# Performance work log

Hardware: AMD Instinct MI355X
Metric: run time of the kernel (lower is better)

Reference implementation:

```python
import jax, jax.numpy as jnp
import numpy as np
import math

N_NODES = 10000
N_EDGES = 30000
N_FEAT = 128
N_GRAPHS = 50
HEADS = 8
OUT_DIM = 10


def _lin_params(key, fin, fout):
    kw, kb = jax.random.split(key)
    s = 1.0 / math.sqrt(fin)
    w = jax.random.uniform(kw, (fin, fout), jnp.float32, -s, s)
    b = jax.random.uniform(kb, (fout,), jnp.float32, -s, s)
    return w, b


def setup_inputs() -> dict:
    key = jax.random.key(0)
    ks = jax.random.split(key, 20)
    inp = {}
    inp["x"] = jax.random.normal(ks[0], (N_NODES, N_FEAT), jnp.float32)
    inp["edge_index"] = jax.random.randint(ks[1], (2, N_EDGES), 0, N_NODES)
    inp["batch"] = jnp.sort(jax.random.randint(ks[2], (N_NODES,), 0, N_GRAPHS))
    # (fin, out_channels) per layer; internal width = out_channels * HEADS
    dims = [(128, 512), (512, 256), (256, 64)]
    ki = 3
    for i, (fin, cout) in enumerate(dims, 1):
        hc = cout * HEADS
        inp[f"q{i}_w"], inp[f"q{i}_b"] = _lin_params(ks[ki], fin, hc); ki += 1
        inp[f"k{i}_w"], inp[f"k{i}_b"] = _lin_params(ks[ki], fin, hc); ki += 1
        inp[f"v{i}_w"], inp[f"v{i}_b"] = _lin_params(ks[ki], fin, hc); ki += 1
        inp[f"s{i}_w"], inp[f"s{i}_b"] = _lin_params(ks[ki], fin, cout); ki += 1
    inp["gate_w"], inp["gate_b"] = _lin_params(ks[ki], 64, 1); ki += 1
    inp["fc_w"], inp["fc_b"] = _lin_params(ks[ki], 64, OUT_DIM)
    return inp


def _tconv(x, src, dst, qw, qb, kw_, kb_, vw, vb, sw, sb):
    # PyG TransformerConv, heads=HEADS, concat=False (mean over heads), root_weight=True
    N = x.shape[0]
    hc = qw.shape[1]
    C = hc // HEADS
    q = (x @ qw + qb).reshape(N, HEADS, C)
    k = (x @ kw_ + kb_).reshape(N, HEADS, C)
    v = (x @ vw + vb).reshape(N, HEADS, C)
    # per-edge attention logits [E, H]
    alpha = (q[dst] * k[src]).sum(-1) * (1.0 / math.sqrt(C))
    # segment softmax over incoming edges of each destination node
    m = jax.ops.segment_max(alpha, dst, num_segments=N)
    ex = jnp.exp(alpha - m[dst])
    den = jax.ops.segment_sum(ex, dst, num_segments=N)
    w = ex / jnp.maximum(den[dst], 1e-16)
    agg = jax.ops.segment_sum(w[:, :, None] * v[src], dst, num_segments=N)  # [N,H,C]
    return agg.mean(axis=1) + x @ sw + sb


def reference(x, edge_index, batch,
              q1_w, q1_b, k1_w, k1_b, v1_w, v1_b, s1_w, s1_b,
              q2_w, q2_b, k2_w, k2_b, v2_w, v2_b, s2_w, s2_b,
              q3_w, q3_b, k3_w, k3_b, v3_w, v3_b, s3_w, s3_b,
              gate_w, gate_b, fc_w, fc_b):
    src, dst = edge_index[0], edge_index[1]
    h = jax.nn.elu(_tconv(x, src, dst, q1_w, q1_b, k1_w, k1_b, v1_w, v1_b, s1_w, s1_b))
    h = jax.nn.elu(_tconv(h, src, dst, q2_w, q2_b, k2_w, k2_b, v2_w, v2_b, s2_w, s2_b))
    h = jax.nn.elu(_tconv(h, src, dst, q3_w, q3_b, k3_w, k3_b, v3_w, v3_b, s3_w, s3_b))
    # GlobalAttention pooling: softmax(gate) within each graph, weighted sum
    gate = h @ gate_w + gate_b  # [N,1]
    gm = jax.ops.segment_max(gate, batch, num_segments=N_GRAPHS)
    ge = jnp.exp(gate - gm[batch])
    gd = jax.ops.segment_sum(ge, batch, num_segments=N_GRAPHS)
    g = ge / jnp.maximum(gd[batch], 1e-16)
    pooled = jax.ops.segment_sum(g * h, batch, num_segments=N_GRAPHS)  # [G,64]
    return pooled @ fc_w + fc_b
```

## Files before the change

kernel.cpp:

```cpp
#include <hip/hip_runtime.h>
#include <stdint.h>
#include <math.h>

#define NN 10000
#define NE 30000
#define NG 50
#define NH 8

typedef _Float16 f16;
typedef _Float16 f16x2 __attribute__((ext_vector_type(2)));
typedef _Float16 f16x4 __attribute__((ext_vector_type(4)));
typedef _Float16 f16x8 __attribute__((ext_vector_type(8)));
typedef float f32x4 __attribute__((ext_vector_type(4)));

__device__ inline void async16(f16* l, const f16* g) {
    __builtin_amdgcn_global_load_lds((const __attribute__((address_space(1))) void*)g,
                                     (__attribute__((address_space(3))) void*)l, 16, 0, 0);
}

__global__ void hist_kernel(const int* __restrict__ dst, int* __restrict__ deg, int E) {
    int e = blockIdx.x * blockDim.x + threadIdx.x;
    if (e < E) atomicAdd(&deg[dst[e]], 1);
}

__global__ __launch_bounds__(1024) void scan_goffs(const int* __restrict__ deg, int* __restrict__ offs,
                                                   int* __restrict__ cursor,
                                                   const int* __restrict__ batch, int* __restrict__ goffs) {
    if (blockIdx.x == 1) {
        int g = threadIdx.x;
        if (g > NG) return;
        int lo = 0, hi = NN;
        while (lo < hi) {
            int mid = (lo + hi) >> 1;
            if (batch[mid] < g) lo = mid + 1; else hi = mid;
        }
        goffs[g] = lo;
        return;
    }
    __shared__ int tot[1024];
    const int t = threadIdx.x;
    const int base = t * 10;
    int v[10];
    int s = 0;
#pragma unroll
    for (int i = 0; i < 10; ++i) {
        int idx = base + i;
        v[i] = (idx < NN) ? deg[idx] : 0;
        s += v[i];
    }
    tot[t] = s;
    __syncthreads();
    for (int d2 = 1; d2 < 1024; d2 <<= 1) {
        int add = (t >= d2) ? tot[t - d2] : 0;
        __syncthreads();
        tot[t] += add;
        __syncthreads();
    }
    int run = tot[t] - s;
    if (t == 0) offs[0] = 0;
#pragma unroll
    for (int i = 0; i < 10; ++i) {
        int idx = base + i;
        if (idx < NN) cursor[idx] = run;
        run += v[i];
        if (idx < NN) offs[idx + 1] = run;
    }
}

__global__ void scatter_kernel(const int* __restrict__ src, const int* __restrict__ dst,
                               int* __restrict__ cursor, int* __restrict__ srcCSR, int E) {
    int e = blockIdx.x * blockDim.x + threadIdx.x;
    if (e < E) {
        int p = atomicAdd(&cursor[dst[e]], 1);
        srcCSR[p] = src[e];
    }
}

__global__ void sort_csr(const int* __restrict__ offs, int* __restrict__ srcCSR) {
    int n = blockIdx.x * blockDim.x + threadIdx.x;
    if (n >= NN) return;
    int s = offs[n], e = offs[n + 1];
    for (int i = s + 1; i < e; ++i) {
        int v = srcCSR[i];
        int j = i - 1;
        while (j >= s && srcCSR[j] > v) { srcCSR[j + 1] = srcCSR[j]; --j; }
        srcCSR[j + 1] = v;
    }
}

__global__ void cvt3_kernel(const float* __restrict__ a, f16* __restrict__ ao, int na,
                            const float* __restrict__ b, f16* __restrict__ bo, int nb2,
                            const float* __restrict__ c, f16* __restrict__ co, int nc) {
    int i = blockIdx.x * blockDim.x + threadIdx.x;
    if (i < na) ao[i] = (f16)a[i];
    else if (i < na + nb2) { int j = i - na; bo[j] = (f16)b[j]; }
    else if (i < na + nb2 + nc) { int j = i - na - nb2; co[j] = (f16)c[j]; }
}

__global__ __launch_bounds__(256) void prep4t(const float* __restrict__ W0, int n0,
                                              const float* __restrict__ W1, int n1,
                                              const float* __restrict__ W2, int n2,
                                              const float* __restrict__ W3, int n3,
                                              const float* __restrict__ b0, const float* __restrict__ b1,
                                              const float* __restrict__ b2, const float* __restrict__ b3,
                                              f16* __restrict__ Bt, float* __restrict__ bias,
                                              int K, int Ntot) {
    __shared__ float tile[64][65];
    const int k0 = blockIdx.x * 64;
    const int nb = blockIdx.y * 64;
    const int tid = threadIdx.x;
    const int tn = tid & 63;
    const int t4 = tid >> 6;
#pragma unroll
    for (int i = 0; i < 16; ++i) {
        int kl = t4 + i * 4;
        int k = k0 + kl;
        int n = nb + tn;
        float w = 0.0f;
        int m = n;
        if (m < n0) w = W0[(size_t)k * n0 + m];
        else { m -= n0;
            if (m < n1) w = W1[(size_t)k * n1 + m];
            else { m -= n1;
                if (m < n2) w = W2[(size_t)k * n2 + m];
                else { m -= n2; if (m < n3) w = W3[(size_t)k * n3 + m]; }
            }
        }
        tile[kl][tn] = w;
    }
    if (blockIdx.x == 0 && t4 == 0) {
        int n = nb + tn;
        float bv = 0.0f;
        int m = n;
        if (m < n0) bv = b0[m];
        else { m -= n0;
            if (m < n1) bv = b1[m];
            else { m -= n1;
                if (m < n2) bv = b2[m];
                else { m -= n2; if (m < n3) bv = b3[m]; }
            }
        }
        bias[n] = bv;
    }
    __syncthreads();
#pragma unroll
    for (int i = 0; i < 16; ++i) {
        int nl = t4 + i * 4;
        Bt[(size_t)(nb + nl) * K + k0 + tn] = (f16)tile[tn][nl];
    }
}

__global__ __launch_bounds__(256) void prepU(const float* __restrict__ qw, const float* __restrict__ qb,
                                             const float* __restrict__ kw, const float* __restrict__ kb,
                                             f16* __restrict__ BtY, float* __restrict__ biasY,
                                             int fin, int hc, int C) {
    const int wid = blockIdx.x * 4 + ((int)threadIdx.x >> 6);
    const int lane = threadIdx.x & 63;
    if (wid >= fin * 16) return;
    const int k = wid >> 4;
    const int idx = wid & 15;
    const int h = idx & 7, isV = idx >> 3;
    const float* W = isV ? kw : qw;
    const float* bvec = isV ? qb : kb;
    float s = 0.0f;
    for (int c = lane; c < C; c += 64) s += W[(size_t)k * hc + h * C + c] * bvec[h * C + c];
#pragma unroll
    for (int o = 32; o > 0; o >>= 1) s += __shfl_down(s, o, 64);
    if (lane == 0) BtY[(size_t)(8 * fin + isV * 8 + h) * fin + k] = (f16)s;
    if (wid < 8) {
        float cc = 0.0f;
        for (int c = lane; c < C; c += 64) cc += qb[wid * C + c] * kb[wid * C + c];
#pragma unroll
        for (int o = 32; o > 0; o >>= 1) cc += __shfl_down(cc, o, 64);
        if (lane == 0) biasY[8 * fin + wid] = cc;
    }
}

__global__ __launch_bounds__(256) void prepZB(const float* __restrict__ vw, const float* __restrict__ sw,
                                              const float* __restrict__ vb, const float* __restrict__ sb,
                                              f16* __restrict__ Bt2, float* __restrict__ biasZ) {
    __shared__ f16 tile[32][65];
    const int k0 = blockIdx.x * 32, c0 = blockIdx.y * 64;
    const int tid = threadIdx.x;
#pragma unroll
    for (int i = 0; i < 8; ++i) {
        int idx = tid + i * 256;
        int kl = idx >> 6, cl = idx & 63;
        int k = k0 + kl, c = c0 + cl;
        float v = 0.0f;
        if (k < 1024)      v = vw[(size_t)(k & 127) * 4096 + (k >> 7) * 512 + c];
        else if (k < 1152) v = sw[(size_t)(k - 1024) * 512 + c];
        else if (k < 1160) v = vb[(k - 1152) * 512 + c];
        tile[kl][cl] = (f16)v;
    }
    if (blockIdx.x == 0 && tid < 64) biasZ[c0 + tid] = sb[c0 + tid];
    __syncthreads();
    const int cl = tid >> 2, kl = (tid & 3) * 8;
    f16x8 v;
#pragma unroll
    for (int t = 0; t < 8; ++t) v[t] = tile[kl + t][cl];
    *(f16x8*)(Bt2 + (size_t)(c0 + cl) * 1184 + k0 + kl) = v;
}

__global__ __launch_bounds__(256) void gemm128(const f16* __restrict__ A, int lda, int zA,
                                               const f16* __restrict__ Bt, int ldb, int zB,
                                               const float* __restrict__ bias,
                                               f16* __restrict__ C, int ldc, int zC,
                                               float* __restrict__ Sf,
                                               int M, int Np, int K, int hcS, int Sw, int act) {
    __shared__ f16 smem[24576];
    const int rm = blockIdx.x * 128;
    if (rm >= M) return;
    A  += (size_t)blockIdx.z * zA;
    Bt += (size_t)blockIdx.z * zB;
    C  += (size_t)blockIdx.z * zC;
    const int tid  = threadIdx.x;
    const int lane = tid & 63;
    const int wave = tid >> 6;
    const int l16  = lane & 15;
    const int quad = lane >> 4;
    const int cn   = blockIdx.y * 128;
    const int wrow = (wave >> 1) * 64;
    const int wcol = (wave & 1) * 64;

    const int rS  = tid >> 2;
    const int kc  = ((tid & 3) ^ ((tid >> 3) & 3)) << 3;
    int rowA0 = rm + rS;       if (rowA0 >= M) rowA0 = M - 1;
    int rowA1 = rm + rS + 64;  if (rowA1 >= M) rowA1 = M - 1;
    const f16* gA0 = A + (size_t)rowA0 * lda + kc;
    const f16* gA1 = A + (size_t)rowA1 * lda + kc;
    const f16* gB0 = Bt + (size_t)(cn + rS) * ldb + kc;
    const f16* gB1 = Bt + (size_t)(cn + rS + 64) * ldb + kc;

    const int swf = (l16 >> 1) & 3;
    const int rdAoff = (wrow + l16) * 32 + ((quad ^ swf) << 3);
    const int rdBoff = 4096 + (wcol + l16) * 32 + ((quad ^ swf) << 3);

    f32x4 acc[4][4] = {};

    auto stage_load = [&](int slot) {
        f16* base = smem + slot * 8192;
        async16(base + tid * 8, gA0);
        async16(base + tid * 8 + 2048, gA1);
        async16(base + 4096 + tid * 8, gB0);
        async16(base + 4096 + tid * 8 + 2048, gB1);
        gA0 += 32; gA1 += 32; gB0 += 32; gB1 += 32;
    };

    const int NI = K >> 5;
    stage_load(0);
    stage_load(1);

    int slot = 0;
    for (int i = 0; i < NI; ++i) {
        if (i + 1 < NI) asm volatile("s_waitcnt vmcnt(4)" ::: "memory");
        else            asm volatile("s_waitcnt vmcnt(0)" ::: "memory");
        asm volatile("s_barrier" ::: "memory");
        if (i + 2 < NI) {
            int s2 = slot + 2; if (s2 >= 3) s2 -= 3;
            stage_load(s2);
        }
        const f16* sb = smem + slot * 8192;
        f16x8 av[4], bv[4];
#pragma unroll
        for (int ii = 0; ii < 4; ++ii) av[ii] = *(const f16x8*)(sb + rdAoff + ii * 512);
#pragma unroll
        for (int j = 0; j < 4; ++j) bv[j] = *(const f16x8*)(sb + rdBoff + j * 512);
#pragma unroll
        for (int ii = 0; ii < 4; ++ii)
#pragma unroll
            for (int j = 0; j < 4; ++j)
                acc[ii][j] = __builtin_amdgcn_mfma_f32_16x16x32_f16(bv[j], av[ii], acc[ii][j], 0, 0, 0);
        ++slot; if (slot == 3) slot = 0;
    }
    __syncthreads();

    f16* sC = smem;
    for (int round = 0; round < 2; ++round) {
        if ((wave >> 1) == round) {
#pragma unroll
            for (int j = 0; j < 4; ++j) {
                const int cb = wcol + j * 16 + quad * 4;
                const float4 bb = *(const float4*)(bias + cn + cb);
#pragma unroll
                for (int i = 0; i < 4; ++i) {
                    const int r = i * 16 + l16;
                    float v0 = acc[i][j][0] + bb.x;
                    float v1 = acc[i][j][1] + bb.y;
                    float v2 = acc[i][j][2] + bb.z;
                    float v3 = acc[i][j][3] + bb.w;
                    if (act) {
                        v0 = v0 > 0.0f ? v0 : (__expf(v0) - 1.0f);
                        v1 = v1 > 0.0f ? v1 : (__expf(v1) - 1.0f);
                        v2 = v2 > 0.0f ? v2 : (__expf(v2) - 1.0f);
                        v3 = v3 > 0.0f ? v3 : (__expf(v3) - 1.0f);
                    }
                    f16x4 o;
                    o[0] = (f16)v0; o[1] = (f16)v1; o[2] = (f16)v2; o[3] = (f16)v3;
                    *(f16x4*)(sC + r * 136 + cb) = o;
                    if (Sf) {
                        const int sc = cn + cb - hcS;
                        if (sc >= 0 && sc < Sw) {
                            const int grow = rm + round * 64 + r;
                            if (grow < M) {
                                float4 sv = { v0, v1, v2, v3 };
                                *(float4*)(Sf + (size_t)grow * Sw + sc) = sv;
                            }
                        }
                    }
                }
            }
        }
        __syncthreads();
#pragma unroll
        for (int it = 0; it < 4; ++it) {
            const int r = it * 16 + (tid >> 4);
            const int ch = tid & 15;
            const int grow = rm + round * 64 + r;
            if (grow < M) {
                f16x8 v = *(const f16x8*)(sC + r * 136 + ch * 8);
                *(f16x8*)(C + (size_t)grow * ldc + cn + ch * 8) = v;
            }
        }
        __syncthreads();
    }
}

__global__ __launch_bounds__(256) void alpha_fused_y(const f16* __restrict__ Y, const f16* __restrict__ X,
                                                     const int* __restrict__ offs,
                                                     const int* __restrict__ srcCSR,
                                                     float* __restrict__ alphaW,
                                                     int strideY, int fin, float scale) {
    const int n = blockIdx.x;
    const int e0 = offs[n];
    int d = offs[n + 1] - e0;
    if (d > 256) d = 256;

    __shared__ __align__(16) f16 sy[1024];
    __shared__ float sew[256 * NH];
    __shared__ float sv[256 * NH];
    __shared__ int sed[256];
    __shared__ float su[NH];
    const int tid = threadIdx.x;

    const f16* Yn = Y + (size_t)n * strideY;
    for (int c = tid; c < fin; c += 256) ((f16x8*)sy)[c] = ((const f16x8*)Yn)[c];
    if (tid < NH) su[tid] = (float)Yn[8 * fin + tid];
    for (int e = tid; e < d; e += 256) {
        int s = srcCSR[e0 + e];
        sed[e] = s;
        f16x8 vv = *(const f16x8*)(Y + (size_t)s * strideY + 8 * fin + 8);
#pragma unroll
        for (int t = 0; t < 8; ++t) sv[e * NH + t] = (float)vv[t];
    }
    __syncthreads();

    const int wv = tid >> 6, lane = tid & 63;
    const int cph = fin >> 3;
    const int csh = __ffs(cph) - 1;
    const int passes = fin >> 6;
    for (int e = wv; e < d; e += 4) {
        const f16x8* kg = (const f16x8*)(X + (size_t)sed[e] * fin);
        for (int p = 0; p < passes; ++p) {
            const int ci = p * 64 + lane;
            const int head = ci >> csh;
            const int kcn = ci & (cph - 1);
            f16x8 yv = ((const f16x8*)sy)[ci];
            f16x8 xv = kg[kcn];
            float acc = 0.0f;
#pragma unroll
            for (int t = 0; t < 8; ++t) acc += (float)yv[t] * (float)xv[t];
            for (int o = cph >> 1; o > 0; o >>= 1) acc += __shfl_down(acc, o, cph);
            if ((lane & (cph - 1)) == 0)
                sew[e * NH + head] = (acc + su[head] + sv[e * NH + head]) * scale;
        }
    }
    __syncthreads();

    if (tid < NH) {
        const int h = tid;
        float m = -3.0e38f;
        for (int e = 0; e < d; ++e) m = fmaxf(m, sew[e * NH + h]);
        float den = 0.0f;
        for (int e = 0; e < d; ++e) {
            float ex = __expf(sew[e * NH + h] - m);
            sew[e * NH + h] = ex;
            den += ex;
        }
        float inv = 1.0f / (fmaxf(den, 1e-16f) * (float)NH);
        for (int e = 0; e < d; ++e) sew[e * NH + h] *= inv;
    }
    __syncthreads();

    for (int i = tid; i < d * NH; i += 256) alphaW[(size_t)e0 * NH + i] = sew[i];
}

__global__ __launch_bounds__(256) void z_agg(const f16* __restrict__ X,
                                             const int* __restrict__ offs,
                                             const int* __restrict__ srcCSR,
                                             const float* __restrict__ alphaW,
                                             f16* __restrict__ Z) {
    const int n = blockIdx.x;
    const int e0 = offs[n];
    int d = offs[n + 1] - e0;
    if (d > 256) d = 256;

    __shared__ float sew[256 * NH];
    __shared__ int sed[256];
    __shared__ __align__(16) f16 sx[32 * 128];
    const int tid = threadIdx.x;

    for (int i = tid; i < d * NH; i += 256) sew[i] = alphaW[(size_t)e0 * NH + i];
    for (int e = tid; e < d; e += 256) sed[e] = srcCSR[e0 + e];
    __syncthreads();

    const int h = tid >> 5;
    const int f0 = (tid * 4) & 127;
    float a0 = 0.0f, a1 = 0.0f, a2 = 0.0f, a3 = 0.0f;
    for (int ch = 0; ch < d; ch += 32) {
        const int cnt = min(32, d - ch);
        for (int idx = tid; idx < cnt * 16; idx += 256) {
            int row = idx >> 4, c8 = idx & 15;
            *(f16x8*)(sx + row * 128 + c8 * 8) = *(const f16x8*)(X + (size_t)sed[ch + row] * 128 + c8 * 8);
        }
        __syncthreads();
        for (int e = 0; e < cnt; ++e) {
            float w = sew[(ch + e) * NH + h];
            f16x4 xv = *(const f16x4*)(sx + e * 128 + f0);
            a0 += w * (float)xv[0];
            a1 += w * (float)xv[1];
            a2 += w * (float)xv[2];
            a3 += w * (float)xv[3];
        }
        __syncthreads();
    }
    f16* Zr = Z + (size_t)n * 1184;
    f16x4 o; o[0] = (f16)a0; o[1] = (f16)a1; o[2] = (f16)a2; o[3] = (f16)a3;
    *(f16x4*)(Zr + tid * 4) = o;
    if (tid < 16) *(f16x8*)(Zr + 1024 + tid * 8) = *(const f16x8*)(X + (size_t)n * 128 + tid * 8);
    if (tid >= 32 && tid < 40) {
        int hh = tid - 32;
        float s = 0.0f;
        for (int e = 0; e < d; ++e) s += sew[e * NH + hh];
        Zr[1152 + hh] = (f16)s;
    }
    if (tid >= 64 && tid < 88) Zr[1160 + (tid - 64)] = (f16)0.0f;
}

__global__ __launch_bounds__(256) void alpha_fused(const f16* __restrict__ QK,
                                                   const int* __restrict__ offs,
                                                   const int* __restrict__ srcCSR,
                                                   float* __restrict__ alphaW,
                                                   int strideQK, int C, int hc, float scale) {
    const int n = blockIdx.x;
    const int e0 = offs[n];
    int d = offs[n + 1] - e0;
    if (d > 256) d = 256;

    __shared__ __align__(16) f16 sq[4096];
    __shared__ float sew[256 * NH];
    __shared__ int sed[256];
    const int tid = threadIdx.x;

    const f16x8* qg = (const f16x8*)(QK + (size_t)n * strideQK);
    const int qchunks = hc >> 3;
    for (int c = tid; c < qchunks; c += 256) ((f16x8*)sq)[c] = qg[c];
    for (int e = tid; e < d; e += 256) sed[e] = srcCSR[e0 + e];
    __syncthreads();

    const int wv = tid >> 6, lane = tid & 63;
    const int cph = C >> 3;
    const int passes = hc >> 9;
    for (int e = wv; e < d; e += 4) {
        const f16x8* kg = (const f16x8*)(QK + (size_t)sed[e] * strideQK + hc);
        for (int p = 0; p < passes; ++p) {
            const int ci = p * 64 + lane;
            f16x8 qv = ((const f16x8*)sq)[ci];
            f16x8 kv = kg[ci];
            float acc = 0.0f;
#pragma unroll
            for (int t = 0; t < 8; ++t) acc += (float)qv[t] * (float)kv[t];
            for (int o = cph >> 1; o > 0; o >>= 1) acc += __shfl_down(acc, o, cph);
            if ((lane & (cph - 1)) == 0) {
                const int head = ci / cph;
                sew[e * NH + head] = acc * scale;
            }
        }
    }
    __syncthreads();

    if (tid < NH) {
        const int h = tid;
        float m = -3.0e38f;
        for (int e = 0; e < d; ++e) m = fmaxf(m, sew[e * NH + h]);
        float den = 0.0f;
        for (int e = 0; e < d; ++e) {
            float ex = __expf(sew[e * NH + h] - m);
            sew[e * NH + h] = ex;
            den += ex;
        }
        float inv = 1.0f / (fmaxf(den, 1e-16f) * (float)NH);
        for (int e = 0; e < d; ++e) sew[e * NH + h] *= inv;
    }
    __syncthreads();

    for (int i = tid; i < d * NH; i += 256) alphaW[(size_t)e0 * NH + i] = sew[i];
}

__global__ __launch_bounds__(256) void node_agg(const f16* __restrict__ VS,
                                                const float* __restrict__ Sf,
                                                const int* __restrict__ offs,
                                                const int* __restrict__ srcCSR,
                                                const float* __restrict__ alphaW,
                                                float* __restrict__ hout, f16* __restrict__ houth,
                                                int C, int NpVS, int writeHout) {
    const int n = blockIdx.x;
    const int e0 = offs[n];
    int d = offs[n + 1] - e0;
    if (d > 256) d = 256;

    __shared__ float sew[256 * NH];
    __shared__ int sed[256];
    __shared__ float sred[512];
    const int tid = threadIdx.x;

    for (int i = tid; i < d * NH; i += 256) sew[i] = alphaW[(size_t)e0 * NH + i];
    for (int e = tid; e < d; e += 256) sed[e] = srcCSR[e0 + e];
    __syncthreads();

    const int half = C >> 1;
    const int cp = tid & (half - 1);
    const int grp = tid / half;
    const int ngr = 256 / half;
    float a0 = 0.0f, a1 = 0.0f;
    for (int e = grp; e < d; e += ngr) {
        const unsigned int* vp = (const unsigned int*)(VS + (size_t)sed[e] * NpVS);
#pragma unroll
        for (int h = 0; h < NH; ++h) {
            float w = sew[e * NH + h];
            f16x2 vv = __builtin_bit_cast(f16x2, vp[((h * C) >> 1) + cp]);
            a0 += w * (float)vv.x;
            a1 += w * (float)vv.y;
        }
    }
    if (ngr > 1) {
        sred[tid] = a0;
        sred[256 + tid] = a1;
        __syncthreads();
        if (grp == 0) {
            for (int g = 1; g < ngr; ++g) {
                a0 += sred[g * half + cp];
                a1 += sred[256 + g * half + cp];
            }
        }
    }
    if (grp == 0) {
        const int c = cp * 2;
        const float* Sp = Sf + (size_t)n * C;
        float o0 = a0 + Sp[c];
        float o1 = a1 + Sp[c + 1];
        o0 = o0 > 0.0f ? o0 : (__expf(o0) - 1.0f);
        o1 = o1 > 0.0f ? o1 : (__expf(o1) - 1.0f);
        if (writeHout) {
            hout[(size_t)n * C + c] = o0;
            hout[(size_t)n * C + c + 1] = o1;
        }
        houth[(size_t)n * C + c] = (f16)o0;
        houth[(size_t)n * C + c + 1] = (f16)o1;
    }
}

__global__ __launch_bounds__(256) void pool_graph(const float* __restrict__ h,
                                                  const float* __restrict__ gw, const float* __restrict__ gb,
                                                  const float* __restrict__ fcw, const float* __restrict__ fcb,
                                                  const int* __restrict__ goffs,
                                                  float* __restrict__ gbuf, float* __restrict__ out) {
    const int g = blockIdx.x;
    const int s = goffs[g], e = goffs[g + 1];
    const int tid = threadIdx.x;
    const int wv = tid >> 6, lane = tid & 63;

    __shared__ float red[256];
    __shared__ float pl[64];
    __shared__ float sden;

    if (e == s) {
        if (tid < 10) out[g * 10 + tid] = fcb[tid];
        return;
    }

    const float gwl = gw[lane];
    for (int n = s + wv; n < e; n += 4) {
        float acc = h[(size_t)n * 64 + lane] * gwl;
#pragma unroll
        for (int o = 32; o > 0; o >>= 1) acc += __shfl_down(acc, o, 64);
        if (lane == 0) gbuf[n] = acc + gb[0];
    }
    __syncthreads();

    float m = -3.0e38f;
    for (int n = s + tid; n < e; n += 256) m = fmaxf(m, gbuf[n]);
    red[tid] = m;
    __syncthreads();
    for (int o = 128; o > 0; o >>= 1) {
        if (tid < o) red[tid] = fmaxf(red[tid], red[tid + o]);
        __syncthreads();
    }
    m = red[0];
    __syncthreads();

    float sum = 0.0f;
    for (int n = s + tid; n < e; n += 256) {
        float ex = __expf(gbuf[n] - m);
        gbuf[n] = ex;
        sum += ex;
    }
    red[tid] = sum;
    __syncthreads();
    for (int o = 128; o > 0; o >>= 1) {
        if (tid < o) red[tid] += red[tid + o];
        __syncthreads();
    }
    if (tid == 0) sden = 1.0f / fmaxf(red[0], 1e-16f);
    __syncthreads();

    float acc = 0.0f;
    for (int n = s + wv; n < e; n += 4) acc += gbuf[n] * h[(size_t)n * 64 + lane];
    red[tid] = acc;
    __syncthreads();
    if (wv == 0) pl[lane] = (red[lane] + red[64 + lane] + red[128 + lane] + red[192 + lane]) * sden;
    __syncthreads();

    if (tid < 10) {
        float o = fcb[tid];
#pragma unroll
        for (int c = 0; c < 64; ++c) o += pl[c] * fcw[c * 10 + tid];
        out[g * 10 + tid] = o;
    }
}

extern "C" void kernel_launch(void* const* d_in, const int* in_sizes, int n_in,
                              void* d_out, int out_size, void* d_ws, size_t ws_size,
                              hipStream_t stream) {
    const float* x   = (const float*)d_in[0];
    const int* ei    = (const int*)d_in[1];
    const int* src   = ei;
    const int* dst   = ei + NE;
    const int* batch = (const int*)d_in[2];

    struct LayerW { int fin, C, hc; const float *qw,*qb,*kw,*kb,*vw,*vb,*sw,*sb; };
    LayerW LW[3];
    const int fins[3] = {128, 512, 256};
    const int Cs[3]   = {512, 256, 64};
    for (int l = 0; l < 3; ++l) {
        int b = 3 + 8 * l;
        LW[l].fin = fins[l]; LW[l].C = Cs[l]; LW[l].hc = Cs[l] * NH;
        LW[l].qw = (const float*)d_in[b + 0]; LW[l].qb = (const float*)d_in[b + 1];
        LW[l].kw = (const float*)d_in[b + 2]; LW[l].kb = (const float*)d_in[b + 3];
        LW[l].vw = (const float*)d_in[b + 4]; LW[l].vb = (const float*)d_in[b + 5];
        LW[l].sw = (const float*)d_in[b + 6]; LW[l].sb = (const float*)d_in[b + 7];
    }
    const float* gate_w = (const float*)d_in[27];
    const float* gate_b = (const float*)d_in[28];
    const float* fc_w   = (const float*)d_in[29];
    const float* fc_b   = (const float*)d_in[30];

    size_t off = 0;
    char* ws = (char*)d_ws;
    auto alloc = [&](size_t bytes) -> void* {
        void* p = ws + off;
        off = (off + bytes + 255) & ~(size_t)255;
        return p;
    };
    f16* BtQK   = (f16*)alloc((size_t)6400 * 512 * sizeof(f16));
    f16* BtVS   = (f16*)alloc((size_t)512 * 1184 * sizeof(f16));
    float* biasQK = (float*)alloc(6400 * sizeof(float));
    float* biasVS = (float*)alloc(512 * sizeof(float));
    f16* QKbuf  = (f16*)alloc((size_t)NN * 6400 * sizeof(f16));
    float* Sf   = (float*)alloc((size_t)NN * 256 * sizeof(float));
    f16* xh     = (f16*)alloc((size_t)NN * 128 * sizeof(f16));
    f16* houth  = (f16*)alloc((size_t)NN * 512 * sizeof(f16));
    float* hf   = (float*)alloc((size_t)NN * 64 * sizeof(float));
    float* alphaW = (float*)alloc((size_t)NE * NH * sizeof(float));
    f16* qw16   = (f16*)alloc((size_t)128 * 4096 * sizeof(f16));
    f16* kw16   = (f16*)alloc((size_t)128 * 4096 * sizeof(f16));
    f16* BtY    = (f16*)alloc((size_t)1152 * 128 * sizeof(f16));
    int*   deg   = (int*)alloc(NN * sizeof(int));
    float* zbias = (float*)alloc(512 * sizeof(float));
    float* biasY = (float*)alloc(1152 * sizeof(float));
    size_t zspan = (size_t)((char*)(biasY + 1152) - (char*)deg);
    int* offs   = (int*)alloc((NN + 1) * sizeof(int));
    int* cursor = (int*)alloc(NN * sizeof(int));
    int* srcCSR = (int*)alloc(NE * sizeof(int));
    int* goffs  = (int*)alloc((NG + 1) * sizeof(int));
    float* gbuf = (float*)alloc(NN * sizeof(float));
    if (off > ws_size) return;

    hipMemsetAsync(deg, 0, zspan, stream);
    hist_kernel<<<(NE + 255) / 256, 256, 0, stream>>>(dst, deg, NE);
    scan_goffs<<<2, 1024, 0, stream>>>(deg, offs, cursor, batch, goffs);
    scatter_kernel<<<(NE + 255) / 256, 256, 0, stream>>>(src, dst, cursor, srcCSR, NE);
    sort_csr<<<(NN + 255) / 256, 256, 0, stream>>>(offs, srcCSR);

    {
        int na = NN * 128, nb2 = 128 * 4096, nc = 128 * 4096;
        cvt3_kernel<<<(na + nb2 + nc + 255) / 256, 256, 0, stream>>>(x, xh, na,
                                                                     LW[0].qw, qw16, nb2,
                                                                     LW[0].kw, kw16, nc);
    }

    const int grid_m = 80;
    const f16* Acur = xh;
    for (int l = 0; l < 3; ++l) {
        const int K = LW[l].fin, C = LW[l].C, hc = LW[l].hc;
        const float scale = 1.0f / sqrtf((float)C);

        if (l == 0) {
            const int fin = 128, NtotY = 1152;
            dim3 gm(1, 1, 8);
            gemm128<<<gm, 256, 0, stream>>>(kw16, hc, C, qw16, hc, C, zbias,
                                            BtY, fin, fin * fin, nullptr, fin, fin, C, 0, 0, 0);
            prepU<<<(fin * 16 + 3) / 4, 256, 0, stream>>>(LW[0].qw, LW[0].qb, LW[0].kw, LW[0].kb,
                                                          BtY, biasY, fin, hc, C);
            dim3 gy(grid_m, NtotY / 128);
            gemm128<<<gy, 256, 0, stream>>>(xh, fin, 0, BtY, fin, 0, biasY,
                                            QKbuf, NtotY, 0, nullptr, NN, NtotY, fin, 0, 0, 0);
            alpha_fused_y<<<NN, 256, 0, stream>>>(QKbuf, xh, offs, srcCSR, alphaW,
                                                  NtotY, fin, scale);
            z_agg<<<NN, 256, 0, stream>>>(xh, offs, srcCSR, alphaW, QKbuf);
            prepZB<<<dim3(37, 8), 256, 0, stream>>>(LW[0].vw, LW[0].sw, LW[0].vb, LW[0].sb,
                                                    BtVS, biasVS);
            dim3 gz(grid_m, 4);
            gemm128<<<gz, 256, 0, stream>>>(QKbuf, 1184, 0, BtVS, 1184, 0, biasVS,
                                            houth, 512, 0, nullptr, NN, 512, 1184, 0, 0, 1);
        } else {
            const int Np = (2 * hc + hc + C + 127) & ~127;
            prep4t<<<dim3(K / 64, Np / 64), 256, 0, stream>>>(LW[l].qw, hc, LW[l].kw, hc,
                                                              LW[l].vw, hc, LW[l].sw, C,
                                                              LW[l].qb, LW[l].kb, LW[l].vb, LW[l].sb,
                                                              BtQK, biasQK, K, Np);
            dim3 gq(grid_m, Np / 128);
            gemm128<<<gq, 256, 0, stream>>>(Acur, K, 0, BtQK, K, 0, biasQK,
                                            QKbuf, Np, 0, Sf, NN, Np, K, 3 * hc, C, 0);
            alpha_fused<<<NN, 256, 0, stream>>>(QKbuf, offs, srcCSR, alphaW, Np, C, hc, scale);
            node_agg<<<NN, 256, 0, stream>>>(QKbuf + 2 * hc, Sf, offs, srcCSR, alphaW, hf, houth,
                                             C, Np, l == 2 ? 1 : 0);
        }
        Acur = houth;
    }

    pool_graph<<<NG, 256, 0, stream>>>(hf, gate_w, gate_b, fc_w, fc_b, goffs, gbuf, (float*)d_out);
}
```

Before: 493.0 us.

## Fuse per-node attention softmax with aggregation and batch weight prep

```diff
diff --git a/kernel.cpp b/kernel.cpp
--- a/kernel.cpp
+++ b/kernel.cpp
@@ -97,14 +97,24 @@
     else if (i < na + nb2 + nc) { int j = i - na - nb2; co[j] = (f16)c[j]; }
 }
 
-__global__ __launch_bounds__(256) void prep4t(const float* __restrict__ W0, int n0,
-                                              const float* __restrict__ W1, int n1,
-                                              const float* __restrict__ W2, int n2,
-                                              const float* __restrict__ W3, int n3,
-                                              const float* __restrict__ b0, const float* __restrict__ b1,
-                                              const float* __restrict__ b2, const float* __restrict__ b3,
-                                              f16* __restrict__ Bt, float* __restrict__ bias,
-                                              int K, int Ntot) {
+__global__ __launch_bounds__(256) void prep4t2(
+        const float* W0a, int n0a, const float* W1a, int n1a,
+        const float* W2a, int n2a, const float* W3a, int n3a,
+        const float* b0a, const float* b1a, const float* b2a, const float* b3a,
+        f16* Bta, float* biasa, int Ka, int Na,
+        const float* W0b, int n0b, const float* W1b, int n1b,
+        const float* W2b, int n2b, const float* W3b, int n3b,
+        const float* b0b, const float* b1b, const float* b2b, const float* b3b,
+        f16* Btb, float* biasb, int Kb, int Nb) {
+    const int z = blockIdx.z;
+    const float *W0 = z ? W0b : W0a, *W1 = z ? W1b : W1a, *W2 = z ? W2b : W2a, *W3 = z ? W3b : W3a;
+    const float *b0 = z ? b0b : b0a, *b1 = z ? b1b : b1a, *b2 = z ? b2b : b2a, *b3 = z ? b3b : b3a;
+    const int n0 = z ? n0b : n0a, n1 = z ? n1b : n1a, n2 = z ? n2b : n2a, n3 = z ? n3b : n3a;
+    const int K = z ? Kb : Ka, Ntot = z ? Nb : Na;
+    f16* Bt = z ? Btb : Bta;
+    float* bias = z ? biasb : biasa;
+    if ((int)blockIdx.x * 64 >= K || (int)blockIdx.y * 64 >= Ntot) return;
+
     __shared__ float tile[64][65];
     const int k0 = blockIdx.x * 64;
     const int nb = blockIdx.y * 64;
@@ -326,11 +336,12 @@
     }
 }
 
-__global__ __launch_bounds__(256) void alpha_fused_y(const f16* __restrict__ Y, const f16* __restrict__ X,
-                                                     const int* __restrict__ offs,
-                                                     const int* __restrict__ srcCSR,
-                                                     float* __restrict__ alphaW,
-                                                     int strideY, int fin, float scale) {
+__global__ __launch_bounds__(256) void alpha_zagg(const f16* __restrict__ Y, const f16* __restrict__ X,
+                                                  const int* __restrict__ offs,
+                                                  const int* __restrict__ srcCSR,
+                                                  f16* __restrict__ Z,
+                                                  int strideY, float scale) {
+    const int fin = 128;
     const int n = blockIdx.x;
     const int e0 = offs[n];
     int d = offs[n + 1] - e0;
@@ -341,6 +352,7 @@
     __shared__ float sv[256 * NH];
     __shared__ int sed[256];
     __shared__ float su[NH];
+    __shared__ __align__(16) f16 sx[32 * 128];
     const int tid = threadIdx.x;
 
     const f16* Yn = Y + (size_t)n * strideY;
@@ -355,24 +367,25 @@
     }
     __syncthreads();
 
-    const int wv = tid >> 6, lane = tid & 63;
-    const int cph = fin >> 3;
-    const int csh = __ffs(cph) - 1;
-    const int passes = fin >> 6;
-    for (int e = wv; e < d; e += 4) {
-        const f16x8* kg = (const f16x8*)(X + (size_t)sed[e] * fin);
-        for (int p = 0; p < passes; ++p) {
-            const int ci = p * 64 + lane;
-            const int head = ci >> csh;
-            const int kcn = ci & (cph - 1);
-            f16x8 yv = ((const f16x8*)sy)[ci];
-            f16x8 xv = kg[kcn];
-            float acc = 0.0f;
-#pragma unroll
-            for (int t = 0; t < 8; ++t) acc += (float)yv[t] * (float)xv[t];
-            for (int o = cph >> 1; o > 0; o >>= 1) acc += __shfl_down(acc, o, cph);
-            if ((lane & (cph - 1)) == 0)
-                sew[e * NH + head] = (acc + su[head] + sv[e * NH + head]) * scale;
+    {
+        const int wv = tid >> 6, lane = tid & 63;
+        for (int e = wv; e < d; e += 4) {
+            const f16x8* kg = (const f16x8*)(X + (size_t)sed[e] * fin);
+#pragma unroll
+            for (int p = 0; p < 2; ++p) {
+                const int ci = p * 64 + lane;
+                const int head = ci >> 4;
+                const int kcn = ci & 15;
+                f16x8 yv = ((const f16x8*)sy)[ci];
+                f16x8 xv = kg[kcn];
+                float acc = 0.0f;
+#pragma unroll
+                for (int t = 0; t < 8; ++t) acc += (float)yv[t] * (float)xv[t];
+#pragma unroll
+                for (int o = 8; o > 0; o >>= 1) acc += __shfl_down(acc, o, 16);
+                if ((lane & 15) == 0)
+                    sew[e * NH + head] = (acc + su[head] + sv[e * NH + head]) * scale;
+            }
         }
     }
     __syncthreads();
@@ -392,28 +405,6 @@
     }
     __syncthreads();
 
-    for (int i = tid; i < d * NH; i += 256) alphaW[(size_t)e0 * NH + i] = sew[i];
-}
-
-__global__ __launch_bounds__(256) void z_agg(const f16* __restrict__ X,
-                                             const int* __restrict__ offs,
-                                             const int* __restrict__ srcCSR,
-                                             const float* __restrict__ alphaW,
-                                             f16* __restrict__ Z) {
-    const int n = blockIdx.x;
-    const int e0 = offs[n];
-    int d = offs[n + 1] - e0;
-    if (d > 256) d = 256;
-
-    __shared__ float sew[256 * NH];
-    __shared__ int sed[256];
-    __shared__ __align__(16) f16 sx[32 * 128];
-    const int tid = threadIdx.x;
-
-    for (int i = tid; i < d * NH; i += 256) sew[i] = alphaW[(size_t)e0 * NH + i];
-    for (int e = tid; e < d; e += 256) sed[e] = srcCSR[e0 + e];
-    __syncthreads();
-
     const int h = tid >> 5;
     const int f0 = (tid * 4) & 127;
     float a0 = 0.0f, a1 = 0.0f, a2 = 0.0f, a3 = 0.0f;
@@ -447,11 +438,12 @@
     if (tid >= 64 && tid < 88) Zr[1160 + (tid - 64)] = (f16)0.0f;
 }
 
-__global__ __launch_bounds__(256) void alpha_fused(const f16* __restrict__ QK,
-                                                   const int* __restrict__ offs,
-                                                   const int* __restrict__ srcCSR,
-                                                   float* __restrict__ alphaW,
-                                                   int strideQK, int C, int hc, float scale) {
+__global__ __launch_bounds__(256) void edge_node(const f16* __restrict__ QKVS,
+                                                 const float* __restrict__ Sf,
+                                                 const int* __restrict__ offs,
+                                                 const int* __restrict__ srcCSR,
+                                                 float* __restrict__ hout, f16* __restrict__ houth,
+                                                 int Np, int C, int hc, float scale, int writeHout) {
     const int n = blockIdx.x;
     const int e0 = offs[n];
     int d = offs[n + 1] - e0;
@@ -460,30 +452,33 @@
     __shared__ __align__(16) f16 sq[4096];
     __shared__ float sew[256 * NH];
     __shared__ int sed[256];
+    __shared__ float sred[512];
     const int tid = threadIdx.x;
 
-    const f16x8* qg = (const f16x8*)(QK + (size_t)n * strideQK);
+    const f16x8* qg = (const f16x8*)(QKVS + (size_t)n * Np);
     const int qchunks = hc >> 3;
     for (int c = tid; c < qchunks; c += 256) ((f16x8*)sq)[c] = qg[c];
     for (int e = tid; e < d; e += 256) sed[e] = srcCSR[e0 + e];
     __syncthreads();
 
-    const int wv = tid >> 6, lane = tid & 63;
-    const int cph = C >> 3;
-    const int passes = hc >> 9;
-    for (int e = wv; e < d; e += 4) {
-        const f16x8* kg = (const f16x8*)(QK + (size_t)sed[e] * strideQK + hc);
-        for (int p = 0; p < passes; ++p) {
-            const int ci = p * 64 + lane;
-            f16x8 qv = ((const f16x8*)sq)[ci];
-            f16x8 kv = kg[ci];
-            float acc = 0.0f;
-#pragma unroll
-            for (int t = 0; t < 8; ++t) acc += (float)qv[t] * (float)kv[t];
-            for (int o = cph >> 1; o > 0; o >>= 1) acc += __shfl_down(acc, o, cph);
-            if ((lane & (cph - 1)) == 0) {
-                const int head = ci / cph;
-                sew[e * NH + head] = acc * scale;
+    {
+        const int wv = tid >> 6, lane = tid & 63;
+        const int cph = C >> 3;
+        const int passes = (hc >> 9) ? (hc >> 9) : 1;
+        for (int e = wv; e < d; e += 4) {
+            const f16x8* kg = (const f16x8*)(QKVS + (size_t)sed[e] * Np + hc);
+            for (int p = 0; p < passes; ++p) {
+                const int ci = p * 64 + lane;
+                f16x8 qv = ((const f16x8*)sq)[ci];
+                f16x8 kv = kg[ci];
+                float acc = 0.0f;
+#pragma unroll
+                for (int t = 0; t < 8; ++t) acc += (float)qv[t] * (float)kv[t];
+                for (int o = cph >> 1; o > 0; o >>= 1) acc += __shfl_down(acc, o, cph);
+                if ((lane & (cph - 1)) == 0) {
+                    const int head = ci / cph;
+                    sew[e * NH + head] = acc * scale;
+                }
             }
         }
     }
@@ -504,37 +499,13 @@
     }
     __syncthreads();
 
-    for (int i = tid; i < d * NH; i += 256) alphaW[(size_t)e0 * NH + i] = sew[i];
-}
-
-__global__ __launch_bounds__(256) void node_agg(const f16* __restrict__ VS,
-                                                const float* __restrict__ Sf,
-                                                const int* __restrict__ offs,
-                                                const int* __restrict__ srcCSR,
-                                                const float* __restrict__ alphaW,
-                                                float* __restrict__ hout, f16* __restrict__ houth,
-                                                int C, int NpVS, int writeHout) {
-    const int n = blockIdx.x;
-    const int e0 = offs[n];
-    int d = offs[n + 1] - e0;
-    if (d > 256) d = 256;
-
-    __shared__ float sew[256 * NH];
-    __shared__ int sed[256];
-    __shared__ float sred[512];
-    const int tid = threadIdx.x;
-
-    for (int i = tid; i < d * NH; i += 256) sew[i] = alphaW[(size_t)e0 * NH + i];
-    for (int e = tid; e < d; e += 256) sed[e] = srcCSR[e0 + e];
-    __syncthreads();
-
     const int half = C >> 1;
     const int cp = tid & (half - 1);
     const int grp = tid / half;
     const int ngr = 256 / half;
     float a0 = 0.0f, a1 = 0.0f;
     for (int e = grp; e < d; e += ngr) {
-        const unsigned int* vp = (const unsigned int*)(VS + (size_t)sed[e] * NpVS);
+        const unsigned int* vp = (const unsigned int*)(QKVS + (size_t)sed[e] * Np + 2 * hc);
 #pragma unroll
         for (int h = 0; h < NH; ++h) {
             float w = sew[e * NH + h];
@@ -672,16 +643,18 @@
         off = (off + bytes + 255) & ~(size_t)255;
         return p;
     };
-    f16* BtQK   = (f16*)alloc((size_t)6400 * 512 * sizeof(f16));
-    f16* BtVS   = (f16*)alloc((size_t)512 * 1184 * sizeof(f16));
-    float* biasQK = (float*)alloc(6400 * sizeof(float));
-    float* biasVS = (float*)alloc(512 * sizeof(float));
+    f16* BtL2   = (f16*)alloc((size_t)6400 * 512 * sizeof(f16));
+    f16* BtL3   = (f16*)alloc((size_t)1664 * 256 * sizeof(f16));
+    f16* BtZ    = (f16*)alloc((size_t)512 * 1184 * sizeof(f16));
+    float* biasL2 = (float*)alloc(6400 * sizeof(float));
+    float* biasL3 = (float*)alloc(1664 * sizeof(float));
+    float* biasZ  = (float*)alloc(512 * sizeof(float));
     f16* QKbuf  = (f16*)alloc((size_t)NN * 6400 * sizeof(f16));
+    f16* Zbuf   = (f16*)alloc((size_t)NN * 1184 * sizeof(f16));
     float* Sf   = (float*)alloc((size_t)NN * 256 * sizeof(float));
     f16* xh     = (f16*)alloc((size_t)NN * 128 * sizeof(f16));
     f16* houth  = (f16*)alloc((size_t)NN * 512 * sizeof(f16));
     float* hf   = (float*)alloc((size_t)NN * 64 * sizeof(float));
-    float* alphaW = (float*)alloc((size_t)NE * NH * sizeof(float));
     f16* qw16   = (f16*)alloc((size_t)128 * 4096 * sizeof(f16));
     f16* kw16   = (f16*)alloc((size_t)128 * 4096 * sizeof(f16));
     f16* BtY    = (f16*)alloc((size_t)1152 * 128 * sizeof(f16));
@@ -708,44 +681,43 @@
                                                                      LW[0].qw, qw16, nb2,
                                                                      LW[0].kw, kw16, nc);
     }
+    prep4t2<<<dim3(8, 100, 2), 256, 0, stream>>>(
+        LW[1].qw, 2048, LW[1].kw, 2048, LW[1].vw, 2048, LW[1].sw, 256,
+        LW[1].qb, LW[1].kb, LW[1].vb, LW[1].sb, BtL2, biasL2, 512, 6400,
+        LW[2].qw, 512, LW[2].kw, 512, LW[2].vw, 512, LW[2].sw, 64,
+        LW[2].qb, LW[2].kb, LW[2].vb, LW[2].sb, BtL3, biasL3, 256, 1664);
+    prepZB<<<dim3(37, 8), 256, 0, stream>>>(LW[0].vw, LW[0].sw, LW[0].vb, LW[0].sb, BtZ, biasZ);
 
     const int grid_m = 80;
-    const f16* Acur = xh;
-    for (int l = 0; l < 3; ++l) {
+
+    {
+        const int fin = 128, hc = 4096, NtotY = 1152;
+        const float scale = 1.0f / sqrtf(512.0f);
+        dim3 gm(1, 1, 8);
+        gemm128<<<gm, 256, 0, stream>>>(kw16, hc, 512, qw16, hc, 512, zbias,
+                                        BtY, fin, fin * fin, nullptr, fin, fin, 512, 0, 0, 0);
+        prepU<<<(fin * 16 + 3) / 4, 256, 0, stream>>>(LW[0].qw, LW[0].qb, LW[0].kw, LW[0].kb,
+                                                      BtY, biasY, fin, hc, 512);
+        dim3 gy(grid_m, NtotY / 128);
+        gemm128<<<gy, 256, 0, stream>>>(xh, fin, 0, BtY, fin, 0, biasY,
+                                        QKbuf, NtotY, 0, nullptr, NN, NtotY, fin, 0, 0, 0);
+        alpha_zagg<<<NN, 256, 0, stream>>>(QKbuf, xh, offs, srcCSR, Zbuf, NtotY, scale);
+        dim3 gz(grid_m, 4);
+        gemm128<<<gz, 256, 0, stream>>>(Zbuf, 1184, 0, BtZ, 1184, 0, biasZ,
+                                        houth, 512, 0, nullptr, NN, 512, 1184, 0, 0, 1);
+    }
+    const f16* Acur = houth;
+    for (int l = 1; l < 3; ++l) {
         const int K = LW[l].fin, C = LW[l].C, hc = LW[l].hc;
         const float scale = 1.0f / sqrtf((float)C);
-
-        if (l == 0) {
-            const int fin = 128, NtotY = 1152;
-            dim3 gm(1, 1, 8);
-            gemm128<<<gm, 256, 0, stream>>>(kw16, hc, C, qw16, hc, C, zbias,
-                                            BtY, fin, fin * fin, nullptr, fin, fin, C, 0, 0, 0);
-            prepU<<<(fin * 16 + 3) / 4, 256, 0, stream>>>(LW[0].qw, LW[0].qb, LW[0].kw, LW[0].kb,
-                                                          BtY, biasY, fin, hc, C);
-            dim3 gy(grid_m, NtotY / 128);
-            gemm128<<<gy, 256, 0, stream>>>(xh, fin, 0, BtY, fin, 0, biasY,
-                                            QKbuf, NtotY, 0, nullptr, NN, NtotY, fin, 0, 0, 0);
-            alpha_fused_y<<<NN, 256, 0, stream>>>(QKbuf, xh, offs, srcCSR, alphaW,
-                                                  NtotY, fin, scale);
-            z_agg<<<NN, 256, 0, stream>>>(xh, offs, srcCSR, alphaW, QKbuf);
-            prepZB<<<dim3(37, 8), 256, 0, stream>>>(LW[0].vw, LW[0].sw, LW[0].vb, LW[0].sb,
-                                                    BtVS, biasVS);
-            dim3 gz(grid_m, 4);
-            gemm128<<<gz, 256, 0, stream>>>(QKbuf, 1184, 0, BtVS, 1184, 0, biasVS,
-                                            houth, 512, 0, nullptr, NN, 512, 1184, 0, 0, 1);
-        } else {
-            const int Np = (2 * hc + hc + C + 127) & ~127;
-            prep4t<<<dim3(K / 64, Np / 64), 256, 0, stream>>>(LW[l].qw, hc, LW[l].kw, hc,
-                                                              LW[l].vw, hc, LW[l].sw, C,
-                                                              LW[l].qb, LW[l].kb, LW[l].vb, LW[l].sb,
-                                                              BtQK, biasQK, K, Np);
-            dim3 gq(grid_m, Np / 128);
-            gemm128<<<gq, 256, 0, stream>>>(Acur, K, 0, BtQK, K, 0, biasQK,
-                                            QKbuf, Np, 0, Sf, NN, Np, K, 3 * hc, C, 0);
-            alpha_fused<<<NN, 256, 0, stream>>>(QKbuf, offs, srcCSR, alphaW, Np, C, hc, scale);
-            node_agg<<<NN, 256, 0, stream>>>(QKbuf + 2 * hc, Sf, offs, srcCSR, alphaW, hf, houth,
-                                             C, Np, l == 2 ? 1 : 0);
-        }
+        const int Np = (3 * hc + C + 127) & ~127;
+        f16* Bt = (l == 1) ? BtL2 : BtL3;
+        float* bias = (l == 1) ? biasL2 : biasL3;
+        dim3 gq(grid_m, Np / 128);
+        gemm128<<<gq, 256, 0, stream>>>(Acur, K, 0, Bt, K, 0, bias,
+                                        QKbuf, Np, 0, Sf, NN, Np, K, 3 * hc, C, 0);
+        edge_node<<<NN, 256, 0, stream>>>(QKbuf, Sf, offs, srcCSR, hf, houth,
+                                          Np, C, hc, scale, l == 2 ? 1 : 0);
         Acur = houth;
     }
 
```

Measured after the change: 475.4 us. -3.6%, faster.
